# Kernel tuning notes

Measured on AMD Instinct MI355X. Metric: run time of the kernel, lower is better.

The kernel has to match this reference:

```python
import jax, jax.numpy as jnp
import numpy as np

NEG_INF = -9e15  # matches the -9000000000000000.0 mask constant in the torch code
ALPHA = 0.2      # LeakyReLU negative slope


def setup_inputs() -> dict:
    key = jax.random.key(0)
    ks = jax.random.split(key, 8)
    N, F = 8192, 256
    h = jax.random.normal(ks[0], (N, F), dtype=jnp.float32)
    adj = jax.random.randint(ks[1], (N, N), 0, 2).astype(jnp.float32)
    W = jax.random.normal(ks[2], (F, F), dtype=jnp.float32) * 0.05
    a = jax.random.normal(ks[3], (2 * F, 1), dtype=jnp.float32) * 0.05
    w_ih = jax.random.normal(ks[4], (3 * F, F), dtype=jnp.float32) * 0.05
    w_hh = jax.random.normal(ks[5], (3 * F, F), dtype=jnp.float32) * 0.05
    b_ih = jax.random.normal(ks[6], (3 * F,), dtype=jnp.float32) * 0.05
    b_hh = jax.random.normal(ks[7], (3 * F,), dtype=jnp.float32) * 0.05
    return {"h": h, "adj": adj, "W": W, "a": a,
            "w_ih": w_ih, "w_hh": w_hh, "b_ih": b_ih, "b_hh": b_hh}


def reference(h, adj, W, a, w_ih, w_hh, b_ih, b_hh):
    F_out = W.shape[1]
    Wh = h @ W  # [N, F]
    # a_input @ a decomposes exactly: e_ij = leakyrelu(Wh_i . a[:F] + Wh_j . a[F:])
    src = Wh @ a[:F_out]   # [N, 1]
    dst = Wh @ a[F_out:]   # [N, 1]
    e = jax.nn.leaky_relu(src + dst.T, ALPHA)          # [N, N]
    att = jnp.where(adj > 0, e, NEG_INF)
    att = jax.nn.softmax(att, axis=1)                   # dropout: eval mode (identity)
    h_prime = att @ Wh                                  # [N, F]
    # torch GRUCell(h_prime, h)
    gi = h_prime @ w_ih.T + b_ih                        # [N, 3F]
    gh = h @ w_hh.T + b_hh
    i_r, i_z, i_n = jnp.split(gi, 3, axis=1)
    h_r, h_z, h_n = jnp.split(gh, 3, axis=1)
    r = jax.nn.sigmoid(i_r + h_r)
    z = jax.nn.sigmoid(i_z + h_z)
    n = jnp.tanh(i_n + r * h_n)
    return (1.0 - z) * n + z * h
```

## Files before the change

kernel.cpp:

```cpp
#include <hip/hip_runtime.h>

typedef __attribute__((ext_vector_type(8))) short bf16x8;
typedef __attribute__((ext_vector_type(4))) float f32x4;
typedef unsigned short u16;
typedef unsigned int u32;

#define NN 8192
#define FD 256

__device__ __forceinline__ u16 f2bf(float f) {
  union { float f; unsigned u; } v; v.f = f;
  unsigned r = v.u + 0x7FFF + ((v.u >> 16) & 1);
  return (u16)(r >> 16);
}

__device__ __forceinline__ bf16x8 ldcvt8(const float* __restrict__ p) {
  f32x4 x0 = *(const f32x4*)p;
  f32x4 x1 = *(const f32x4*)(p + 4);
  bf16x8 t;
  t[0] = (short)f2bf(x0[0]); t[1] = (short)f2bf(x0[1]);
  t[2] = (short)f2bf(x0[2]); t[3] = (short)f2bf(x0[3]);
  t[4] = (short)f2bf(x1[0]); t[5] = (short)f2bf(x1[1]);
  t[6] = (short)f2bf(x1[2]); t[7] = (short)f2bf(x1[3]);
  return t;
}

__device__ __forceinline__ void gl16(const void* g, void* l) {
  __builtin_amdgcn_global_load_lds((const __attribute__((address_space(1))) u32*)g,
                                   (__attribute__((address_space(3))) u32*)l, 16, 0, 0);
}

__global__ __launch_bounds__(256) void k_zero(float* __restrict__ p) {
  int g = (blockIdx.x * 256 + threadIdx.x) * 4;
  f32x4 z = {0.f, 0.f, 0.f, 0.f};
  *(f32x4*)(p + g) = z;
}

__global__ __launch_bounds__(256) void k_wh(const float* __restrict__ h,
                                            const float* __restrict__ W,
                                            const float* __restrict__ a,
                                            u16* __restrict__ whT,
                                            float* __restrict__ src,
                                            float* __restrict__ dst) {
  int tid = threadIdx.x;
  int lane = tid & 63;
  int wv = tid >> 6;
  int r0 = blockIdx.x * 64 + (wv >> 1) * 32;
  int c0 = blockIdx.y * 64 + (wv & 1) * 32;
  int lr = lane & 15;
  int q = lane >> 4;

  f32x4 acc[2][2] = {};
  for (int kk = 0; kk < FD; kk += 32) {
    int kb = kk + q * 8;
    bf16x8 av[2], bv[2];
#pragma unroll
    for (int m = 0; m < 2; m++)
      av[m] = ldcvt8(h + (size_t)(r0 + m * 16 + lr) * FD + kb);
#pragma unroll
    for (int n = 0; n < 2; n++) {
      int col = c0 + n * 16 + lr;
      const float* p = W + (size_t)kb * FD + col;
      bf16x8 t;
#pragma unroll
      for (int e = 0; e < 8; e++) t[e] = (short)f2bf(p[(size_t)e * FD]);
      bv[n] = t;
    }
#pragma unroll
    for (int m = 0; m < 2; m++)
#pragma unroll
      for (int n = 0; n < 2; n++)
        acc[m][n] = __builtin_amdgcn_mfma_f32_16x16x32_bf16(av[m], bv[n], acc[m][n], 0, 0, 0);
  }
#pragma unroll
  for (int m = 0; m < 2; m++)
#pragma unroll
    for (int n = 0; n < 2; n++) {
      int gc = c0 + n * 16 + lr;
      int gr = r0 + m * 16 + q * 4;
      ushort4 st;
      st.x = f2bf(acc[m][n][0]);
      st.y = f2bf(acc[m][n][1]);
      st.z = f2bf(acc[m][n][2]);
      st.w = f2bf(acc[m][n][3]);
      *(ushort4*)(whT + (size_t)gc * NN + gr) = st;
    }
  float aA0 = a[c0 + lr], aA1 = a[c0 + 16 + lr];
  float aB0 = a[256 + c0 + lr], aB1 = a[256 + c0 + 16 + lr];
#pragma unroll
  for (int m = 0; m < 2; m++)
#pragma unroll
    for (int j = 0; j < 4; j++) {
      float s1 = acc[m][0][j] * aA0 + acc[m][1][j] * aA1;
      float s2 = acc[m][0][j] * aB0 + acc[m][1][j] * aB1;
#pragma unroll
      for (int sh = 1; sh < 16; sh <<= 1) {
        s1 += __shfl_xor(s1, sh);
        s2 += __shfl_xor(s2, sh);
      }
      if (lr == 0) {
        int row = r0 + m * 16 + q * 4 + j;
        atomicAdd(&src[row], s1);
        atomicAdd(&dst[row], s2);
      }
    }
}

__global__ __launch_bounds__(512, 2) void k_att(const float* __restrict__ adj,
                                                const u16* __restrict__ whT,
                                                const float* __restrict__ src,
                                                const float* __restrict__ dst,
                                                float* __restrict__ hpp,
                                                float* __restrict__ lgp) {
  __shared__ u16 wtile[4][8192];
  __shared__ u16 pbuf[2][10240];
  __shared__ float dst_lds[1024];

  const int tid = threadIdx.x;
  const int lane = tid & 63;
  const int w = tid >> 6;
  const int lr = lane & 15;
  const int q = lane >> 4;
  const int rg = w >> 1;
  const int ch = w & 1;
  const int bid = blockIdx.x;
  const int jh = bid & 7;
  const int i0 = (bid >> 3) * 256;
  const int jb = jh * 1024;

  const int pr = tid >> 1;
  const int pj = (tid & 1) * 16;
  const float* adjP = adj + (size_t)(i0 + pr) * NN + jb + pj;
  const float srcv = src[i0 + pr];

  const int gcr = lane >> 2;
  const int jsw = (lane & 3) ^ (gcr & 3);
  const u16* wsrc0 = whT + (size_t)(w * 32 + gcr) * NN + jb + jsw * 8;
  const u16* wsrc1 = wsrc0 + (size_t)16 * NN;

  f32x4 acc[4][8] = {};
  float lsum = 0.f;
  f32x4 arE[4], arO[4];

#define GLDS(T)                                                              \
  {                                                                          \
    int _s = (T) & 3;                                                        \
    gl16(wsrc0 + (size_t)((T) & 31) * 32, &wtile[_s][w * 1024]);             \
    gl16(wsrc1 + (size_t)((T) & 31) * 32, &wtile[_s][w * 1024 + 512]);       \
  }
#define ALD(T, AR)                                                           \
  { _Pragma("unroll") for (int v = 0; v < 4; v++)                            \
      AR[v] = *(const f32x4*)(adjP + (size_t)((T) & 31) * 32 + v * 4); }
#define PGEN(T, AR, PB)                                                      \
  {                                                                          \
    _Pragma("unroll") for (int v = 0; v < 4; v++) {                          \
      f32x4 dv = *(const f32x4*)&dst_lds[((T) & 31) * 32 + pj + v * 4];      \
      ushort4 st;                                                            \
      { float x = srcv + dv[0]; x = fmaxf(x, 0.2f * x); float p = AR[v][0] * __expf(x); lsum += p; st.x = f2bf(p); } \
      { float x = srcv + dv[1]; x = fmaxf(x, 0.2f * x); float p = AR[v][1] * __expf(x); lsum += p; st.y = f2bf(p); } \
      { float x = srcv + dv[2]; x = fmaxf(x, 0.2f * x); float p = AR[v][2] * __expf(x); lsum += p; st.z = f2bf(p); } \
      { float x = srcv + dv[3]; x = fmaxf(x, 0.2f * x); float p = AR[v][3] * __expf(x); lsum += p; st.w = f2bf(p); } \
      *(ushort4*)&pbuf[PB][pr * 40 + pj + v * 4] = st;                       \
    }                                                                        \
  }
#define MSTEP(T, PB)                                                         \
  {                                                                          \
    const u16* bb = &wtile[(T) & 3][0];                                      \
    const u16* pp = &pbuf[PB][0];                                            \
    bf16x8 bfs[8];                                                           \
    _Pragma("unroll") for (int ct = 0; ct < 8; ct++)                         \
      bfs[ct] = *(const bf16x8*)&bb[(ch * 4 + (ct >> 1)) * 1024 + (ct & 1) * 512 + lr * 32 + (q ^ (lr & 3)) * 8]; \
    __builtin_amdgcn_s_setprio(1);                                           \
    _Pragma("unroll") for (int rt = 0; rt < 4; rt++) {                       \
      bf16x8 af = *(const bf16x8*)&pp[(rg * 64 + rt * 16 + lr) * 40 + q * 8]; \
      _Pragma("unroll") for (int ct = 0; ct < 8; ct++)                       \
        acc[rt][ct] = __builtin_amdgcn_mfma_f32_16x16x32_bf16(af, bfs[ct], acc[rt][ct], 0, 0, 0); \
    }                                                                        \
    __builtin_amdgcn_s_setprio(0);                                           \
  }
#define ENDBAR asm volatile("s_waitcnt vmcnt(10) lgkmcnt(0)\n\ts_barrier" ::: "memory")

  if (tid < 256) {
    f32x4 v = *(const f32x4*)(dst + jb + tid * 4);
    *(f32x4*)&dst_lds[tid * 4] = v;
  }
  GLDS(0);
  GLDS(1);
  ALD(0, arE);
  ALD(1, arO);
  __syncthreads();
  PGEN(0, arE, 0);
  ALD(2, arE);
  asm volatile("s_waitcnt lgkmcnt(0)\n\ts_barrier" ::: "memory");

  for (int t = 0; t < 32; t += 2) {
    GLDS(t + 2);
    PGEN(t + 1, arO, 1);
    ALD(t + 3, arO);
    MSTEP(t, 0);
    ENDBAR;
    GLDS(t + 3);
    PGEN(t + 2, arE, 0);
    ALD(t + 4, arE);
    MSTEP(t + 1, 1);
    ENDBAR;
  }
#undef GLDS
#undef ALD
#undef PGEN
#undef MSTEP
#undef ENDBAR

  lsum += __shfl_xor(lsum, 1);
  if ((lane & 1) == 0) lgp[jh * NN + i0 + pr] = lsum;

  float* hs = hpp + (size_t)jh * NN * FD;
#pragma unroll
  for (int rt = 0; rt < 4; rt++)
#pragma unroll
    for (int ct = 0; ct < 8; ct++) {
      int c = ch * 128 + ct * 16 + lr;
#pragma unroll
      for (int j = 0; j < 4; j++) {
        int row = i0 + rg * 64 + rt * 16 + q * 4 + j;
        hs[(size_t)row * FD + c] = acc[rt][ct][j];
      }
    }
}

__global__ __launch_bounds__(256) void k_norm(const float* __restrict__ hpp,
                                              const float* __restrict__ lgp,
                                              u16* __restrict__ hpb) {
  int gid = blockIdx.x * 256 + threadIdx.x;
  int idx = gid * 4;
  int row = idx >> 8;
  f32x4 s = {0.f, 0.f, 0.f, 0.f};
  float l = 0.f;
#pragma unroll
  for (int jh = 0; jh < 8; jh++) {
    s += *(const f32x4*)(hpp + (size_t)jh * NN * FD + idx);
    l += lgp[jh * NN + row];
  }
  float inv = 1.0f / l;
  ushort4 st;
  st.x = f2bf(s[0] * inv);
  st.y = f2bf(s[1] * inv);
  st.z = f2bf(s[2] * inv);
  st.w = f2bf(s[3] * inv);
  *(ushort4*)(hpb + idx) = st;
}

__global__ __launch_bounds__(256) void k_gru(const u16* __restrict__ hpb,
                                             const float* __restrict__ h,
                                             const float* __restrict__ wih,
                                             const float* __restrict__ whh,
                                             const float* __restrict__ bih,
                                             const float* __restrict__ bhh,
                                             float* __restrict__ out) {
  int tid = threadIdx.x;
  int lane = tid & 63;
  int wv = tid >> 6;
  int i0 = blockIdx.x * 32;
  int lr = lane & 15;
  int q = lane >> 4;
  int c = blockIdx.y * 64 + wv * 16 + lr;
  f32x4 gi[3][2] = {};
  f32x4 gh[3][2] = {};
  for (int kk = 0; kk < FD; kk += 32) {
    int kb = kk + q * 8;
    bf16x8 ap[2], ah[2], bi[3], bh[3];
#pragma unroll
    for (int m = 0; m < 2; m++) {
      ap[m] = *(const bf16x8*)(hpb + (size_t)(i0 + m * 16 + lr) * FD + kb);
      ah[m] = ldcvt8(h + (size_t)(i0 + m * 16 + lr) * FD + kb);
    }
#pragma unroll
    for (int g = 0; g < 3; g++) {
      bi[g] = ldcvt8(wih + (size_t)(g * 256 + c) * FD + kb);
      bh[g] = ldcvt8(whh + (size_t)(g * 256 + c) * FD + kb);
    }
#pragma unroll
    for (int g = 0; g < 3; g++)
#pragma unroll
      for (int m = 0; m < 2; m++) {
        gi[g][m] = __builtin_amdgcn_mfma_f32_16x16x32_bf16(ap[m], bi[g], gi[g][m], 0, 0, 0);
        gh[g][m] = __builtin_amdgcn_mfma_f32_16x16x32_bf16(ah[m], bh[g], gh[g][m], 0, 0, 0);
      }
  }
  float bir = bih[c], biz = bih[256 + c], bin = bih[512 + c];
  float bhr = bhh[c], bhz = bhh[256 + c], bhn = bhh[512 + c];
#pragma unroll
  for (int m = 0; m < 2; m++)
#pragma unroll
    for (int j = 0; j < 4; j++) {
      int row = i0 + m * 16 + q * 4 + j;
      float rv = gi[0][m][j] + bir + gh[0][m][j] + bhr;
      float zv = gi[1][m][j] + biz + gh[1][m][j] + bhz;
      float r = 1.f / (1.f + __expf(-rv));
      float z = 1.f / (1.f + __expf(-zv));
      float nx = gi[2][m][j] + bin + r * (gh[2][m][j] + bhn);
      float n = 1.f - 2.f / (__expf(2.f * nx) + 1.f);
      float hv = h[(size_t)row * FD + c];
      out[(size_t)row * FD + c] = (1.f - z) * n + z * hv;
    }
}

extern "C" void kernel_launch(void* const* d_in, const int* in_sizes, int n_in,
                              void* d_out, int out_size, void* d_ws, size_t ws_size,
                              hipStream_t stream) {
  const float* h   = (const float*)d_in[0];
  const float* adj = (const float*)d_in[1];
  const float* W   = (const float*)d_in[2];
  const float* a   = (const float*)d_in[3];
  const float* wih = (const float*)d_in[4];
  const float* whh = (const float*)d_in[5];
  const float* bih = (const float*)d_in[6];
  const float* bhh = (const float*)d_in[7];
  float* out = (float*)d_out;

  char* ws = (char*)d_ws;
  u16* whT   = (u16*)(ws);
  u16* hpb   = (u16*)(ws);
  float* hpp = (float*)(ws + 4194304);
  float* lgp = (float*)(ws + 71303168);
  float* srcv = (float*)(ws + 71565312);
  float* dstv = (float*)(ws + 71598080);
  (void)ws_size;

  k_zero<<<16, 256, 0, stream>>>(srcv);
  k_wh<<<dim3(128, 4), 256, 0, stream>>>(h, W, a, whT, srcv, dstv);
  k_att<<<256, 512, 0, stream>>>(adj, whT, srcv, dstv, hpp, lgp);
  k_norm<<<2048, 256, 0, stream>>>(hpp, lgp, hpb);
  k_gru<<<dim3(256, 4), 256, 0, stream>>>(hpb, h, wih, whh, bih, bhh, out);
}
```

Before: 208.0 us.

## Pack adjacency into bitmask in a pre-pass and consume bits in attention kernel

Adds a k_bits kernel that streams the fp32 adjacency matrix once and packs nonzero flags into 32-bit words. The attention kernel then loads one u32 per 32 columns instead of sixteen floats per thread-step, and selects exp(x) or zero from the bits. The vmcnt wait is lowered to match the fewer outstanding loads. The full adjacency still has to be read once in the new pass. That costs an extra launch and a small bitmask round trip, in exchange for freeing k_att's memory pipeline and registers for the MFMA loop.

```diff
diff --git a/kernel.cpp b/kernel.cpp
--- a/kernel.cpp
+++ b/kernel.cpp
@@ -34,6 +34,22 @@
   int g = (blockIdx.x * 256 + threadIdx.x) * 4;
   f32x4 z = {0.f, 0.f, 0.f, 0.f};
   *(f32x4*)(p + g) = z;
+}
+
+__global__ __launch_bounds__(256) void k_bits(const float* __restrict__ adj,
+                                              u32* __restrict__ bits) {
+  size_t g = (size_t)blockIdx.x * 256 + threadIdx.x;
+  const float* p = adj + g * 32;
+  u32 w = 0;
+#pragma unroll
+  for (int v = 0; v < 8; v++) {
+    f32x4 x = *(const f32x4*)(p + v * 4);
+    w |= (x[0] != 0.f ? 1u : 0u) << (v * 4);
+    w |= (x[1] != 0.f ? 1u : 0u) << (v * 4 + 1);
+    w |= (x[2] != 0.f ? 1u : 0u) << (v * 4 + 2);
+    w |= (x[3] != 0.f ? 1u : 0u) << (v * 4 + 3);
+  }
+  bits[g] = w;
 }
 
 __global__ __launch_bounds__(256) void k_wh(const float* __restrict__ h,
@@ -106,7 +122,7 @@
     }
 }
 
-__global__ __launch_bounds__(512, 2) void k_att(const float* __restrict__ adj,
+__global__ __launch_bounds__(512, 2) void k_att(const u32* __restrict__ bits,
                                                 const u16* __restrict__ whT,
                                                 const float* __restrict__ src,
                                                 const float* __restrict__ dst,
@@ -130,7 +146,7 @@
 
   const int pr = tid >> 1;
   const int pj = (tid & 1) * 16;
-  const float* adjP = adj + (size_t)(i0 + pr) * NN + jb + pj;
+  const u32* bp = bits + (size_t)(i0 + pr) * 256 + jh * 32;
   const float srcv = src[i0 + pr];
 
   const int gcr = lane >> 2;
@@ -140,7 +156,7 @@
 
   f32x4 acc[4][8] = {};
   float lsum = 0.f;
-  f32x4 arE[4], arO[4];
+  u32 wE, wO;
 
 #define GLDS(T)                                                              \
   {                                                                          \
@@ -148,18 +164,17 @@
     gl16(wsrc0 + (size_t)((T) & 31) * 32, &wtile[_s][w * 1024]);             \
     gl16(wsrc1 + (size_t)((T) & 31) * 32, &wtile[_s][w * 1024 + 512]);       \
   }
-#define ALD(T, AR)                                                           \
-  { _Pragma("unroll") for (int v = 0; v < 4; v++)                            \
-      AR[v] = *(const f32x4*)(adjP + (size_t)((T) & 31) * 32 + v * 4); }
-#define PGEN(T, AR, PB)                                                      \
+#define BITLD(T, R) R = bp[(T) & 31];
+#define PGEN(T, R, PB)                                                       \
   {                                                                          \
+    u32 wv = (R) >> pj;                                                      \
     _Pragma("unroll") for (int v = 0; v < 4; v++) {                          \
       f32x4 dv = *(const f32x4*)&dst_lds[((T) & 31) * 32 + pj + v * 4];      \
       ushort4 st;                                                            \
-      { float x = srcv + dv[0]; x = fmaxf(x, 0.2f * x); float p = AR[v][0] * __expf(x); lsum += p; st.x = f2bf(p); } \
-      { float x = srcv + dv[1]; x = fmaxf(x, 0.2f * x); float p = AR[v][1] * __expf(x); lsum += p; st.y = f2bf(p); } \
-      { float x = srcv + dv[2]; x = fmaxf(x, 0.2f * x); float p = AR[v][2] * __expf(x); lsum += p; st.z = f2bf(p); } \
-      { float x = srcv + dv[3]; x = fmaxf(x, 0.2f * x); float p = AR[v][3] * __expf(x); lsum += p; st.w = f2bf(p); } \
+      { float x = srcv + dv[0]; x = fmaxf(x, 0.2f * x); float p = ((wv >> (v * 4)) & 1) ? __expf(x) : 0.f; lsum += p; st.x = f2bf(p); } \
+      { float x = srcv + dv[1]; x = fmaxf(x, 0.2f * x); float p = ((wv >> (v * 4 + 1)) & 1) ? __expf(x) : 0.f; lsum += p; st.y = f2bf(p); } \
+      { float x = srcv + dv[2]; x = fmaxf(x, 0.2f * x); float p = ((wv >> (v * 4 + 2)) & 1) ? __expf(x) : 0.f; lsum += p; st.z = f2bf(p); } \
+      { float x = srcv + dv[3]; x = fmaxf(x, 0.2f * x); float p = ((wv >> (v * 4 + 3)) & 1) ? __expf(x) : 0.f; lsum += p; st.w = f2bf(p); } \
       *(ushort4*)&pbuf[PB][pr * 40 + pj + v * 4] = st;                       \
     }                                                                        \
   }
@@ -178,7 +193,7 @@
     }                                                                        \
     __builtin_amdgcn_s_setprio(0);                                           \
   }
-#define ENDBAR asm volatile("s_waitcnt vmcnt(10) lgkmcnt(0)\n\ts_barrier" ::: "memory")
+#define ENDBAR asm volatile("s_waitcnt vmcnt(4) lgkmcnt(0)\n\ts_barrier" ::: "memory")
 
   if (tid < 256) {
     f32x4 v = *(const f32x4*)(dst + jb + tid * 4);
@@ -186,27 +201,27 @@
   }
   GLDS(0);
   GLDS(1);
-  ALD(0, arE);
-  ALD(1, arO);
+  BITLD(0, wE);
+  BITLD(1, wO);
   __syncthreads();
-  PGEN(0, arE, 0);
-  ALD(2, arE);
+  PGEN(0, wE, 0);
+  BITLD(2, wE);
   asm volatile("s_waitcnt lgkmcnt(0)\n\ts_barrier" ::: "memory");
 
   for (int t = 0; t < 32; t += 2) {
     GLDS(t + 2);
-    PGEN(t + 1, arO, 1);
-    ALD(t + 3, arO);
+    PGEN(t + 1, wO, 1);
+    BITLD(t + 3, wO);
     MSTEP(t, 0);
     ENDBAR;
     GLDS(t + 3);
-    PGEN(t + 2, arE, 0);
-    ALD(t + 4, arE);
+    PGEN(t + 2, wE, 0);
+    BITLD(t + 4, wE);
     MSTEP(t + 1, 1);
     ENDBAR;
   }
 #undef GLDS
-#undef ALD
+#undef BITLD
 #undef PGEN
 #undef MSTEP
 #undef ENDBAR
@@ -325,11 +340,13 @@
   float* lgp = (float*)(ws + 71303168);
   float* srcv = (float*)(ws + 71565312);
   float* dstv = (float*)(ws + 71598080);
+  u32* bits  = (u32*)(ws + 71630848);
   (void)ws_size;
 
   k_zero<<<16, 256, 0, stream>>>(srcv);
+  k_bits<<<8192, 256, 0, stream>>>(adj, bits);
   k_wh<<<dim3(128, 4), 256, 0, stream>>>(h, W, a, whT, srcv, dstv);
-  k_att<<<256, 512, 0, stream>>>(adj, whT, srcv, dstv, hpp, lgp);
+  k_att<<<256, 512, 0, stream>>>(bits, whT, srcv, dstv, hpp, lgp);
   k_norm<<<2048, 256, 0, stream>>>(hpp, lgp, hpb);
   k_gru<<<dim3(256, 4), 256, 0, stream>>>(hpb, h, wih, whh, bih, bhh, out);
 }
```

Measured after the change: 220.9 us. 6.2% more time.
